# Kernel tuning notes

Hardware: AMD Instinct MI355X
Metric: run time of the kernel (lower is better)

## Reference

```python
import jax, jax.numpy as jnp
import numpy as np


def _rule_stack(x_q):
    # x_q: [B, 2, 4]; a/b are the two context panels, per attribute column -> [B, 4]
    a = x_q[:, 0, :]
    b = x_q[:, 1, :]
    # 13 fixed rules applied elementwise across the 4 attribute columns -> [B, 4, 13]
    return jnp.stack([
        a,
        b - 2.0, b - 1.0, b + 1.0, b + 2.0,
        a - b, a + b,
        jnp.minimum(a, b), jnp.maximum(a, b),
        b + 2.0, b + 1.0, b - 2.0, b - 1.0,
    ], axis=-1)


def setup_inputs() -> dict:
    key = jax.random.key(0)
    k1, k2, k3, k4 = jax.random.split(key, 4)
    B, Z = 262144, 512
    z = jax.random.normal(k1, (B, Z), dtype=jnp.float32)
    x_q = jax.random.normal(k2, (B, 2, 4), dtype=jnp.float32)
    # rule_encoder: Linear(z_dim -> 4*13)
    W = jax.random.normal(k3, (Z, 52), dtype=jnp.float32) / np.sqrt(Z)
    b = jax.random.normal(k4, (52,), dtype=jnp.float32) * 0.01
    return {"z": z, "x_q": x_q, "W": W, "b": b}


def reference(z, x_q, W, b):
    logits = (z @ W + b).reshape(-1, 4, 13)          # [B, 4, 13]
    rule_probs = jax.nn.softmax(logits, axis=-1)       # [B, 4, 13]
    rules = _rule_stack(x_q)                           # [B, 4, 13]
    y_q = jnp.sum(rules * rule_probs, axis=-1)         # [B, 4]
    return y_q[:, None, :]                             # [B, 1, 4]
```

## Files before the change

### kernel.cpp

```cpp
#include <hip/hip_runtime.h>
#include <stdint.h>

typedef __bf16 bf16_t;
typedef bf16_t bf16x8 __attribute__((ext_vector_type(8)));
typedef float f32x2 __attribute__((ext_vector_type(2)));
typedef float f32x4 __attribute__((ext_vector_type(4)));
typedef uint32_t u32x4 __attribute__((ext_vector_type(4)));
typedef uint16_t u16x8 __attribute__((ext_vector_type(8)));

union FragU { u32x4 u; bf16x8 v; u16x8 s; };

__device__ __forceinline__ uint16_t f2bf_rne(float f) {
  uint32_t u = __float_as_uint(f);
  return (uint16_t)((u + 0x7fffu + ((u >> 16) & 1u)) >> 16);
}

__global__ __launch_bounds__(256) void pack_w_kernel(
    const float* __restrict__ W, u32x4* __restrict__ wf) {
  int idx = blockIdx.x * 256 + threadIdx.x;
  if (idx >= 4096) return;
  int lane = idx & 63;
  int nt   = (idx >> 6) & 3;
  int ks   = idx >> 8;
  int n  = nt * 16 + (lane & 15);
  int kb = ks * 32 + (lane >> 4) * 8;
  FragU hi;
#pragma unroll
  for (int j = 0; j < 8; ++j) {
    float w = (n < 52) ? W[(kb + j) * 52 + n] : 0.0f;
    hi.s[j] = f2bf_rne(w);
  }
  wf[idx] = hi.u;
}

#define MFMA16(a, b, c) __builtin_amdgcn_mfma_f32_16x16x32_bf16((a), (b), (c), 0, 0, 0)

__global__ __launch_bounds__(256, 2) void raven_main_kernel(
    const float* __restrict__ z, const float* __restrict__ xq,
    const u32x4* __restrict__ wfh,
    const float* __restrict__ bias, float* __restrict__ out) {
  __shared__ __align__(16) unsigned char smem[65536];
  __shared__ float lds_bias[52];

  const int tid  = threadIdx.x;
  const int wave = tid >> 6;
  const int lane = tid & 63;
  const int r  = lane & 15;
  const int kg = lane >> 4;

  if (tid < 52) lds_bias[tid] = bias[tid];

  const long long brow = (long long)blockIdx.x * 128;
  const long long wrow = brow + (long long)wave * 32;
  const float* zb = z + wrow * 512;

  unsigned char* stg = smem + wave * 16384;

  const int rloc4 = lane >> 4;
  const int slot  = lane & 15;

  f32x4 acc[2][4];
#pragma unroll
  for (int mt = 0; mt < 2; ++mt)
#pragma unroll
    for (int nt = 0; nt < 4; ++nt) {
      f32x4 zv = {0.0f, 0.0f, 0.0f, 0.0f};
      acc[mt][nt] = zv;
    }

#define STAGE_CHUNK(ks_, buf_)                                                  \
  {                                                                             \
    _Pragma("unroll")                                                           \
    for (int i_ = 0; i_ < 8; ++i_) {                                            \
      const int srow_ = i_ * 4 + rloc4;                                         \
      const int foff_ = 4 * (slot ^ (srow_ & 7));                               \
      const float* g_ = zb + srow_ * 512 + (ks_) * 64 + foff_;                  \
      __builtin_amdgcn_global_load_lds(                                         \
          (const __attribute__((address_space(1))) void*)g_,                    \
          (__attribute__((address_space(3))) void*)((buf_) + i_ * 1024),        \
          16, 0, 0);                                                            \
    }                                                                           \
  }

#define LOADB(ks_, set_)                                                        \
  {                                                                             \
    const u32x4* p0_ = wfh + (2 * (ks_)) * 256 + lane;                          \
    const u32x4* p1_ = wfh + (2 * (ks_) + 1) * 256 + lane;                      \
    _Pragma("unroll")                                                           \
    for (int nt_ = 0; nt_ < 4; ++nt_) {                                         \
      bh[set_][nt_].u     = p0_[nt_ * 64];                                      \
      bh[set_][4 + nt_].u = p1_[nt_ * 64];                                      \
    }                                                                           \
  }

  FragU bh[2][8];

  LOADB(0, 0);
  STAGE_CHUNK(0, stg);
  LOADB(1, 1);
  STAGE_CHUNK(1, stg + 8192);

  const int swz = (r & 7) << 4;

#pragma unroll
  for (int ks = 0; ks < 8; ++ks) {
    unsigned char* cur = stg + (ks & 1) * 8192;

    if (ks < 7) asm volatile("s_waitcnt vmcnt(16)" ::: "memory");
    else        asm volatile("s_waitcnt vmcnt(0)"  ::: "memory");
    __builtin_amdgcn_sched_barrier(0);

    FragU h[2][2];
#pragma unroll
    for (int c = 0; c < 2; ++c)
#pragma unroll
      for (int mt = 0; mt < 2; ++mt) {
        const unsigned char* cm = cur + (mt * 16 + r) * 256;
        f32x4 a0 = *(const f32x4*)(cm + ((c * 128 + kg * 32) ^ swz));
        f32x4 a1 = *(const f32x4*)(cm + ((c * 128 + kg * 32 + 16) ^ swz));
#pragma unroll
        for (int j = 0; j < 4; ++j) {
          h[c][mt].v[j]     = (bf16_t)a0[j];
          h[c][mt].v[4 + j] = (bf16_t)a1[j];
        }
      }

    const int cs = ks & 1;
#pragma unroll
    for (int c = 0; c < 2; ++c)
#pragma unroll
      for (int nt = 0; nt < 4; ++nt) {
        acc[0][nt] = MFMA16(h[c][0].v, bh[cs][c * 4 + nt].v, acc[0][nt]);
        acc[1][nt] = MFMA16(h[c][1].v, bh[cs][c * 4 + nt].v, acc[1][nt]);
      }
    __builtin_amdgcn_sched_barrier(0);

    if (ks < 6) {
      LOADB(ks + 2, cs);
      STAGE_CHUNK(ks + 2, cur);
    }
  }
#undef STAGE_CHUNK
#undef LOADB

  __syncthreads();

  float (*lds_t)[132] = (float(*)[132])smem;
#pragma unroll
  for (int mt = 0; mt < 2; ++mt)
#pragma unroll
    for (int nt = 0; nt < 4; ++nt)
      *(f32x4*)&lds_t[nt * 16 + r][wave * 32 + mt * 16 + kg * 4] = acc[mt][nt];

  __syncthreads();

  {
    const int row = tid >> 1;
    const int gp  = (tid & 1) * 2;
    const long long grow = brow + row;
    f32x2 res;
#pragma unroll
    for (int gi = 0; gi < 2; ++gi) {
      const int g = gp + gi;
      float a  = xq[grow * 8 + g];
      float bq = xq[grow * 8 + 4 + g];
      float l[13];
      float m = -1e30f;
#pragma unroll
      for (int u = 0; u < 13; ++u) {
        l[u] = lds_t[g * 13 + u][row] + lds_bias[g * 13 + u];
        m = fmaxf(m, l[u]);
      }
      float s = 0.0f;
#pragma unroll
      for (int u = 0; u < 13; ++u) {
        float e = __expf(l[u] - m);
        l[u] = e;
        s += e;
      }
      float num = a * l[0]
                + (bq - 2.0f) * (l[1] + l[11])
                + (bq - 1.0f) * (l[2] + l[12])
                + (bq + 1.0f) * (l[3] + l[10])
                + (bq + 2.0f) * (l[4] + l[9])
                + (a - bq) * l[5]
                + (a + bq) * l[6]
                + fminf(a, bq) * l[7]
                + fmaxf(a, bq) * l[8];
      res[gi] = num / s;
    }
    *(f32x2*)(out + grow * 4 + gp) = res;
  }
}

extern "C" void kernel_launch(void* const* d_in, const int* in_sizes, int n_in,
                              void* d_out, int out_size, void* d_ws, size_t ws_size,
                              hipStream_t stream) {
  const float* z    = (const float*)d_in[0];
  const float* xq   = (const float*)d_in[1];
  const float* W    = (const float*)d_in[2];
  const float* bias = (const float*)d_in[3];
  float* out = (float*)d_out;

  const int B = in_sizes[0] / 512;

  u32x4* wf = (u32x4*)d_ws;

  hipLaunchKernelGGL(pack_w_kernel, dim3(16), dim3(256), 0, stream, W, wf);

  const int blocks = B / 128;
  hipLaunchKernelGGL(raven_main_kernel, dim3(blocks), dim3(256), 0, stream,
                     z, xq, (const u32x4*)wf, bias, out);
}
```

Baseline: 106.0 us.

## Triple-buffer half-chunk z staging to cut LDS and allow three blocks per CU

Splits each 32-row K-chunk stage into two 16-row half-chunks staged through a three-slot ring buffer per wave, shrinking LDS from 64KB to 48KB per block. Launch bounds are raised to 3 blocks per CU to increase occupancy and memory-level parallelism on the bandwidth-bound z stream. The waitcnt schedule is rewritten for the finer pipeline; the higher occupancy target may constrain registers.

```diff
diff --git a/kernel.cpp b/kernel.cpp
--- a/kernel.cpp
+++ b/kernel.cpp
@@ -35,11 +35,11 @@
 
 #define MFMA16(a, b, c) __builtin_amdgcn_mfma_f32_16x16x32_bf16((a), (b), (c), 0, 0, 0)
 
-__global__ __launch_bounds__(256, 2) void raven_main_kernel(
+__global__ __launch_bounds__(256, 3) void raven_main_kernel(
     const float* __restrict__ z, const float* __restrict__ xq,
     const u32x4* __restrict__ wfh,
     const float* __restrict__ bias, float* __restrict__ out) {
-  __shared__ __align__(16) unsigned char smem[65536];
+  __shared__ __align__(16) unsigned char smem[49152];
   __shared__ float lds_bias[52];
 
   const int tid  = threadIdx.x;
@@ -54,7 +54,7 @@
   const long long wrow = brow + (long long)wave * 32;
   const float* zb = z + wrow * 512;
 
-  unsigned char* stg = smem + wave * 16384;
+  unsigned char* stg = smem + wave * 12288;
 
   const int rloc4 = lane >> 4;
   const int slot  = lane & 15;
@@ -68,79 +68,77 @@
       acc[mt][nt] = zv;
     }
 
-#define STAGE_CHUNK(ks_, buf_)                                                  \
+#define STAGE_HC(p_)                                                            \
+  {                                                                             \
+    unsigned char* b_ = stg + ((p_) % 3) * 4096;                                \
+    const int mt_ = (p_) & 1, ksq_ = (p_) >> 1;                                 \
+    _Pragma("unroll")                                                           \
+    for (int i_ = 0; i_ < 4; ++i_) {                                            \
+      const int srow_ = i_ * 4 + rloc4;                                         \
+      const int foff_ = 4 * (slot ^ (srow_ & 7));                               \
+      const float* g_ = zb + (mt_ * 16 + srow_) * 512 + ksq_ * 64 + foff_;      \
+      __builtin_amdgcn_global_load_lds(                                         \
+          (const __attribute__((address_space(1))) void*)g_,                    \
+          (__attribute__((address_space(3))) void*)(b_ + i_ * 1024),            \
+          16, 0, 0);                                                            \
+    }                                                                           \
+  }
+
+#define LOADB(ks_, set_)                                                        \
   {                                                                             \
     _Pragma("unroll")                                                           \
-    for (int i_ = 0; i_ < 8; ++i_) {                                            \
-      const int srow_ = i_ * 4 + rloc4;                                         \
-      const int foff_ = 4 * (slot ^ (srow_ & 7));                               \
-      const float* g_ = zb + srow_ * 512 + (ks_) * 64 + foff_;                  \
-      __builtin_amdgcn_global_load_lds(                                         \
-          (const __attribute__((address_space(1))) void*)g_,                    \
-          (__attribute__((address_space(3))) void*)((buf_) + i_ * 1024),        \
-          16, 0, 0);                                                            \
+    for (int ksub_ = 0; ksub_ < 2; ++ksub_) {                                   \
+      const u32x4* p_ = wfh + (2 * (ks_) + ksub_) * 256 + lane;                 \
+      _Pragma("unroll")                                                         \
+      for (int nt_ = 0; nt_ < 4; ++nt_)                                         \
+        bh[set_][ksub_ * 4 + nt_].u = p_[nt_ * 64];                             \
     }                                                                           \
   }
 
-#define LOADB(ks_, set_)                                                        \
-  {                                                                             \
-    const u32x4* p0_ = wfh + (2 * (ks_)) * 256 + lane;                          \
-    const u32x4* p1_ = wfh + (2 * (ks_) + 1) * 256 + lane;                      \
-    _Pragma("unroll")                                                           \
-    for (int nt_ = 0; nt_ < 4; ++nt_) {                                         \
-      bh[set_][nt_].u     = p0_[nt_ * 64];                                      \
-      bh[set_][4 + nt_].u = p1_[nt_ * 64];                                      \
-    }                                                                           \
-  }
-
   FragU bh[2][8];
 
   LOADB(0, 0);
-  STAGE_CHUNK(0, stg);
+  STAGE_HC(0);
+  STAGE_HC(1);
   LOADB(1, 1);
-  STAGE_CHUNK(1, stg + 8192);
+  STAGE_HC(2);
 
   const int swz = (r & 7) << 4;
 
 #pragma unroll
-  for (int ks = 0; ks < 8; ++ks) {
-    unsigned char* cur = stg + (ks & 1) * 8192;
-
-    if (ks < 7) asm volatile("s_waitcnt vmcnt(16)" ::: "memory");
-    else        asm volatile("s_waitcnt vmcnt(0)"  ::: "memory");
+  for (int q = 0; q < 16; ++q) {
+    const int ks = q >> 1, mt = q & 1, cs = ks & 1;
+    const unsigned char* buf = stg + (q % 3) * 4096;
+
+    if (q <= 13)      asm volatile("s_waitcnt vmcnt(16)" ::: "memory");
+    else if (q == 14) asm volatile("s_waitcnt vmcnt(4)"  ::: "memory");
+    else              asm volatile("s_waitcnt vmcnt(0)"  ::: "memory");
     __builtin_amdgcn_sched_barrier(0);
 
-    FragU h[2][2];
-#pragma unroll
-    for (int c = 0; c < 2; ++c)
-#pragma unroll
-      for (int mt = 0; mt < 2; ++mt) {
-        const unsigned char* cm = cur + (mt * 16 + r) * 256;
-        f32x4 a0 = *(const f32x4*)(cm + ((c * 128 + kg * 32) ^ swz));
-        f32x4 a1 = *(const f32x4*)(cm + ((c * 128 + kg * 32 + 16) ^ swz));
-#pragma unroll
-        for (int j = 0; j < 4; ++j) {
-          h[c][mt].v[j]     = (bf16_t)a0[j];
-          h[c][mt].v[4 + j] = (bf16_t)a1[j];
-        }
+    const unsigned char* cm = buf + r * 256;
+    FragU h[2];
+#pragma unroll
+    for (int ksub = 0; ksub < 2; ++ksub) {
+      f32x4 a0 = *(const f32x4*)(cm + ((ksub * 128 + kg * 32) ^ swz));
+      f32x4 a1 = *(const f32x4*)(cm + ((ksub * 128 + kg * 32 + 16) ^ swz));
+#pragma unroll
+      for (int j = 0; j < 4; ++j) {
+        h[ksub].v[j]     = (bf16_t)a0[j];
+        h[ksub].v[4 + j] = (bf16_t)a1[j];
       }
-
-    const int cs = ks & 1;
-#pragma unroll
-    for (int c = 0; c < 2; ++c)
-#pragma unroll
-      for (int nt = 0; nt < 4; ++nt) {
-        acc[0][nt] = MFMA16(h[c][0].v, bh[cs][c * 4 + nt].v, acc[0][nt]);
-        acc[1][nt] = MFMA16(h[c][1].v, bh[cs][c * 4 + nt].v, acc[1][nt]);
-      }
+    }
+
+#pragma unroll
+    for (int ksub = 0; ksub < 2; ++ksub)
+#pragma unroll
+      for (int nt = 0; nt < 4; ++nt)
+        acc[mt][nt] = MFMA16(h[ksub].v, bh[cs][ksub * 4 + nt].v, acc[mt][nt]);
     __builtin_amdgcn_sched_barrier(0);
 
-    if (ks < 6) {
-      LOADB(ks + 2, cs);
-      STAGE_CHUNK(ks + 2, cur);
-    }
-  }
-#undef STAGE_CHUNK
+    if (q <= 12) STAGE_HC(q + 3);
+    if ((q & 1) && (ks + 2) <= 7) LOADB(ks + 2, (ks + 2) & 1);
+  }
+#undef STAGE_HC
 #undef LOADB
 
   __syncthreads();
```

Measured after the change: 107.1 us. No clear change (+1.1%).
